# Performance work log

Hardware: AMD Instinct MI355X
Metric: run time of the kernel (lower is better)

The kernel has to match this reference:

```python
import jax, jax.numpy as jnp
import numpy as np

B, N, D, E, R = 4, 4096, 64, 131072, 64

def setup_inputs() -> dict:
    key = jax.random.key(0)
    k1, k2, k3, k4 = jax.random.split(key, 4)
    z = jax.random.normal(k1, (B, N, D), dtype=jnp.float32)
    pairs = jax.random.randint(k2, (E, 2), 0, N, dtype=jnp.int64)
    # Linear params (PyTorch convention: y = x @ W.T + b), init scale ~ 1/sqrt(fan_in)
    W1 = jax.random.normal(k3, (R, 4 * D), dtype=jnp.float32) / np.sqrt(4 * D)
    b1 = jnp.zeros((R,), dtype=jnp.float32)
    W2 = jax.random.normal(k4, (R, R), dtype=jnp.float32) / np.sqrt(R)
    b2 = jnp.zeros((R,), dtype=jnp.float32)
    return {"z": z, "pairs": pairs, "W1": W1, "b1": b1, "W2": W2, "b2": b2}

def reference(z, pairs, W1, b1, W2, b2):
    # gather endpoint embeddings: [B, E, D]
    zi = z[:, pairs[:, 0], :]
    zj = z[:, pairs[:, 1], :]
    # pair feature [B, E, 4D]: concat(zi, zj, zi-zj, zi*zj)
    pair = jnp.concatenate([zi, zj, zi - zj, zi * zj], axis=-1)
    # 2-layer MLP (dropout is identity at inference)
    h = jnp.einsum('bef,rf->ber', pair, W1) + b1
    h = jax.nn.relu(h)
    h = jnp.einsum('ber,sr->bes', h, W2) + b2
    return h
```

## Files before the change

kernel.cpp:

```cpp
#include <hip/hip_runtime.h>
#include <hip/hip_bf16.h>
#include <stdint.h>


typedef __attribute__((ext_vector_type(8))) __bf16 bf16x8;
typedef __attribute__((ext_vector_type(4))) __bf16 bf16x4;
typedef __attribute__((ext_vector_type(4))) float  f32x4;

#define E_TOT 131072
#define N_TOK 4096
#define ROWS_PER_BLOCK 512
#define NSUB 4
#define Z_ELEMS (4 * N_TOK * 64)

__global__ __launch_bounds__(256) void zcast_kernel(const float* __restrict__ z,
                                                    __bf16* __restrict__ zb)
{
    const int t = blockIdx.x * 256 + threadIdx.x;
    const float4 a = ((const float4*)z)[2 * t];
    const float4 b = ((const float4*)z)[2 * t + 1];
    bf16x8 r;
    r[0] = (__bf16)a.x; r[1] = (__bf16)a.y; r[2] = (__bf16)a.z; r[3] = (__bf16)a.w;
    r[4] = (__bf16)b.x; r[5] = (__bf16)b.y; r[6] = (__bf16)b.z; r[7] = (__bf16)b.w;
    ((bf16x8*)zb)[t] = r;
}

__device__ __forceinline__ f32x4 mfma16(bf16x8 a, bf16x8 b, f32x4 c) {
    return __builtin_amdgcn_mfma_f32_16x16x32_bf16(a, b, c, 0, 0, 0);
}

__device__ __forceinline__ bf16x8 pk8(float4 a, float4 b) {
    bf16x8 r;
    r[0] = (__bf16)a.x; r[1] = (__bf16)a.y; r[2] = (__bf16)a.z; r[3] = (__bf16)a.w;
    r[4] = (__bf16)b.x; r[5] = (__bf16)b.y; r[6] = (__bf16)b.z; r[7] = (__bf16)b.w;
    return r;
}
__device__ __forceinline__ float4 f4add(float4 a, float4 b){ return make_float4(a.x+b.x, a.y+b.y, a.z+b.z, a.w+b.w); }
__device__ __forceinline__ float4 f4sub(float4 a, float4 b){ return make_float4(a.x-b.x, a.y-b.y, a.z-b.z, a.w-b.w); }

__device__ __forceinline__ bf16x8 bmul(bf16x8 a, bf16x8 b) {
    bf16x8 r;
#pragma unroll
    for (int t = 0; t < 8; ++t)
        r[t] = (__bf16)((float)a[t] * (float)b[t]);
    return r;
}

__global__ __launch_bounds__(512, 6) void PairRelationEncoder_62775241998442_kernel(
    const __bf16* __restrict__ zw, const int* __restrict__ pairs,
    const float* __restrict__ W1, const float* __restrict__ b1,
    const float* __restrict__ W2, const float* __restrict__ b2,
    float* __restrict__ out)
{
    const int tid  = threadIdx.x;
    const int wave = tid >> 6;
    const int lane = tid & 63;
    const int x = lane & 15;
    const int g = lane >> 4;

    const int bid = (int)(blockIdx.x & 7) * 128 + ((int)blockIdx.x >> 3);
    const int m0 = bid * ROWS_PER_BLOCK;
    const int b  = m0 >> 17;
    const int e0 = m0 & (E_TOT - 1);
    const __bf16* zb = zw + ((size_t)b * N_TOK * 64);

    int2 ijv[NSUB];
#pragma unroll
    for (int st = 0; st < NSUB; ++st)
        ijv[st] = *(const int2*)(pairs + 2 * (size_t)(e0 + (st * 8 + wave) * 16 + x));

    __shared__ __bf16 w1s[64 * 192];
    __shared__ __bf16 w2s[64 * 64];
    __shared__ __bf16 h1s[8][1024];
    __shared__ float  b1s[64];
    __shared__ float  b2s[64];
    __bf16* h1w = h1s[wave];

    {
        const int part = tid >> 7;
        const int scol = tid & 63;
        const int c8b  = ((tid >> 6) & 1) * 4;
        const int cswz = (scol & 7) << 4;
        if (part < 3) {
            const float* wr = W1 + (size_t)scol * 256;
            char* dst = (char*)w1s + scol * 384;
#pragma unroll
            for (int c = 0; c < 4; ++c) {
                const int c8 = c8b + c;
                float4 p0, p1;
                if (part == 0) {
                    float4 a0 = *(const float4*)(wr + c8*8);
                    float4 a1 = *(const float4*)(wr + c8*8 + 4);
                    float4 c0 = *(const float4*)(wr + 128 + c8*8);
                    float4 c1 = *(const float4*)(wr + 128 + c8*8 + 4);
                    p0 = f4add(a0, c0); p1 = f4add(a1, c1);
                } else if (part == 1) {
                    float4 a0 = *(const float4*)(wr + 64 + c8*8);
                    float4 a1 = *(const float4*)(wr + 64 + c8*8 + 4);
                    float4 c0 = *(const float4*)(wr + 128 + c8*8);
                    float4 c1 = *(const float4*)(wr + 128 + c8*8 + 4);
                    p0 = f4sub(a0, c0); p1 = f4sub(a1, c1);
                } else {
                    p0 = *(const float4*)(wr + 192 + c8*8);
                    p1 = *(const float4*)(wr + 192 + c8*8 + 4);
                }
                *(bf16x8*)(dst + ((part * 128 + c8 * 16) ^ cswz)) = pk8(p0, p1);
            }
        } else {
            const float* wr = W2 + (size_t)scol * 64;
            char* dst = (char*)w2s + scol * 128;
#pragma unroll
            for (int c = 0; c < 4; ++c) {
                const int c8 = c8b + c;
                float4 p0 = *(const float4*)(wr + c8*8);
                float4 p1 = *(const float4*)(wr + c8*8 + 4);
                *(bf16x8*)(dst + ((c8 * 16) ^ cswz)) = pk8(p0, p1);
            }
        }
        if (tid < 16)            ((float4*)b1s)[tid]      = ((const float4*)b1)[tid];
        else if (tid < 32)       ((float4*)b2s)[tid - 16] = ((const float4*)b2)[tid - 16];
    }

    __syncthreads();

#pragma unroll
    for (int st = 0; st < NSUB; ++st) {
        const __bf16* zri = zb + (size_t)ijv[st].x * 64;
        const __bf16* zrj = zb + (size_t)ijv[st].y * 64;
        bf16x8 a0 = *(const bf16x8*)(zri + g * 8);
        bf16x8 a1 = *(const bf16x8*)(zri + 32 + g * 8);
        bf16x8 a2 = *(const bf16x8*)(zrj + g * 8);
        bf16x8 a3 = *(const bf16x8*)(zrj + 32 + g * 8);
        bf16x8 a4 = bmul(a0, a2);
        bf16x8 a5 = bmul(a1, a3);

        f32x4 acc[4];
#pragma unroll
        for (int ct = 0; ct < 4; ++ct)
            acc[ct] = *(const f32x4*)(b1s + ct * 16 + g * 4);

#pragma unroll
        for (int h = 0; h < 2; ++h) {
#pragma unroll
            for (int ct = 0; ct < 4; ++ct) {
                const int colr = ct * 16 + x;
                const int cswz = (colr & 7) << 4;
                const char* wb = (const char*)w1s + colr * 384;
                const int kb = h * 64 + g * 16;
                bf16x8 azi = *(const bf16x8*)(wb + ((kb      ) ^ cswz));
                bf16x8 azj = *(const bf16x8*)(wb + ((kb + 128) ^ cswz));
                bf16x8 apr = *(const bf16x8*)(wb + ((kb + 256) ^ cswz));
                acc[ct] = mfma16(azi, (h == 0) ? a0 : a1, acc[ct]);
                acc[ct] = mfma16(azj, (h == 0) ? a2 : a3, acc[ct]);
                acc[ct] = mfma16(apr, (h == 0) ? a4 : a5, acc[ct]);
            }
        }

#pragma unroll
        for (int ct = 0; ct < 4; ++ct) {
            bf16x4 p;
#pragma unroll
            for (int q = 0; q < 4; ++q)
                p[q] = (__bf16)fmaxf(acc[ct][q], 0.f);
            const int wo = (x * 128 + ct * 32 + g * 8) ^ ((x & 7) << 4);
            *(bf16x4*)((char*)h1w + wo) = p;
        }

        f32x4 o[4];
#pragma unroll
        for (int ct = 0; ct < 4; ++ct)
            o[ct] = *(const f32x4*)(b2s + ct * 16 + g * 4);

#pragma unroll
        for (int kk = 0; kk < 2; ++kk) {
            const int aoff = (x * 128 + kk * 64 + g * 16) ^ ((x & 7) << 4);
            const bf16x8 h1f = *(const bf16x8*)((const char*)h1w + aoff);
#pragma unroll
            for (int ct = 0; ct < 4; ++ct) {
                const int cols = ct * 16 + x;
                const bf16x8 w2f = *(const bf16x8*)((const char*)w2s + cols * 128
                                                    + ((kk * 64 + g * 16) ^ ((cols & 7) << 4)));
                o[ct] = mfma16(w2f, h1f, o[ct]);
            }
        }

        float* orow = out + ((size_t)(m0 + (st * 8 + wave) * 16 + x)) * 64;
#pragma unroll
        for (int ct = 0; ct < 4; ++ct)
            *(f32x4*)(orow + ct * 16 + g * 4) = o[ct];
    }
}

extern "C" void kernel_launch(void* const* d_in, const int* in_sizes, int n_in,
                              void* d_out, int out_size, void* d_ws, size_t ws_size,
                              hipStream_t stream) {
    const float* z     = (const float*)d_in[0];
    const int*   pairs = (const int*)  d_in[1];
    const float* W1    = (const float*)d_in[2];
    const float* b1    = (const float*)d_in[3];
    const float* W2    = (const float*)d_in[4];
    const float* b2    = (const float*)d_in[5];
    float* out = (float*)d_out;
    __bf16* zw = (__bf16*)d_ws;

    zcast_kernel<<<Z_ELEMS / (256 * 8), 256, 0, stream>>>(z, zw);

    const int total_rows = 4 * E_TOT;
    dim3 grid(total_rows / ROWS_PER_BLOCK);
    PairRelationEncoder_62775241998442_kernel<<<grid, 512, 0, stream>>>(
        zw, pairs, W1, b1, W2, b2, out);
}
```

Before: 53.72 us.

## Switch to 32x32x16 MFMA tiles and keep layer-1 activations in registers via permlane swap

Replaces the 16x16x32 bf16 MFMA tiling with 32x32x16 tiles, so each wave processes 32 pair rows per sub-step and the number of sub-steps drops from four to two. The ReLU output of layer 1 is packed with v_cvt_pk_bf16_f32 and redistributed across lanes with v_permlane32_swap, so it feeds layer 2 directly as an MFMA operand instead of going through a per-wave LDS buffer. Bias values are stored in LDS in a permuted order to match the 32x32 accumulator layout. This removes the LDS write and read of h1 and reduces per-row W1/W2 fragment reloads, but it raises register use, so the occupancy hint in launch bounds drops from 6 to 4.

```diff
diff --git a/kernel.cpp b/kernel.cpp
--- a/kernel.cpp
+++ b/kernel.cpp
@@ -3,14 +3,15 @@
 #include <stdint.h>
 
 
-typedef __attribute__((ext_vector_type(8))) __bf16 bf16x8;
-typedef __attribute__((ext_vector_type(4))) __bf16 bf16x4;
-typedef __attribute__((ext_vector_type(4))) float  f32x4;
+typedef __attribute__((ext_vector_type(8)))  __bf16 bf16x8;
+typedef __attribute__((ext_vector_type(4)))  float  f32x4;
+typedef __attribute__((ext_vector_type(16))) float  f32x16;
+typedef __attribute__((ext_vector_type(4)))  uint32_t u32x4;
 
 #define E_TOT 131072
 #define N_TOK 4096
 #define ROWS_PER_BLOCK 512
-#define NSUB 4
+#define NSUB 2
 #define Z_ELEMS (4 * N_TOK * 64)
 
 __global__ __launch_bounds__(256) void zcast_kernel(const float* __restrict__ z,
@@ -25,8 +26,8 @@
     ((bf16x8*)zb)[t] = r;
 }
 
-__device__ __forceinline__ f32x4 mfma16(bf16x8 a, bf16x8 b, f32x4 c) {
-    return __builtin_amdgcn_mfma_f32_16x16x32_bf16(a, b, c, 0, 0, 0);
+__device__ __forceinline__ f32x16 mfma32(bf16x8 a, bf16x8 b, f32x16 c) {
+    return __builtin_amdgcn_mfma_f32_32x32x16_bf16(a, b, c, 0, 0, 0);
 }
 
 __device__ __forceinline__ bf16x8 pk8(float4 a, float4 b) {
@@ -46,7 +47,45 @@
     return r;
 }
 
-__global__ __launch_bounds__(512, 6) void PairRelationEncoder_62775241998442_kernel(
+__device__ __forceinline__ uint32_t cvtpk(float lo, float hi) {
+    uint32_t w;
+    asm("v_cvt_pk_bf16_f32 %0, %1, %2" : "=v"(w) : "v"(lo), "v"(hi));
+    return w;
+}
+
+__device__ __forceinline__ void epi(const f32x16 acc, bf16x8& fA, bf16x8& fB) {
+    float v[16];
+#pragma unroll
+    for (int t = 0; t < 16; ++t) v[t] = fmaxf(acc[t], 0.f);
+    uint32_t w00 = cvtpk(v[0],  v[1]);
+    uint32_t w01 = cvtpk(v[2],  v[3]);
+    uint32_t w10 = cvtpk(v[4],  v[5]);
+    uint32_t w11 = cvtpk(v[6],  v[7]);
+    uint32_t w20 = cvtpk(v[8],  v[9]);
+    uint32_t w21 = cvtpk(v[10], v[11]);
+    uint32_t w30 = cvtpk(v[12], v[13]);
+    uint32_t w31 = cvtpk(v[14], v[15]);
+    asm("v_permlane32_swap_b32 %0, %1" : "+v"(w00), "+v"(w10));
+    asm("v_permlane32_swap_b32 %0, %1" : "+v"(w01), "+v"(w11));
+    asm("v_permlane32_swap_b32 %0, %1" : "+v"(w20), "+v"(w30));
+    asm("v_permlane32_swap_b32 %0, %1" : "+v"(w21), "+v"(w31));
+    u32x4 a = {w00, w01, w10, w11};
+    u32x4 b = {w20, w21, w30, w31};
+    fA = __builtin_bit_cast(bf16x8, a);
+    fB = __builtin_bit_cast(bf16x8, b);
+}
+
+__device__ __forceinline__ f32x16 bias_init(const float* tb, int base) {
+    f32x16 a;
+#pragma unroll
+    for (int p = 0; p < 4; ++p) {
+        f32x4 c = *(const f32x4*)(tb + base + 4 * p);
+        a[4*p+0] = c[0]; a[4*p+1] = c[1]; a[4*p+2] = c[2]; a[4*p+3] = c[3];
+    }
+    return a;
+}
+
+__global__ __launch_bounds__(512, 4) void PairRelationEncoder_62775241998442_kernel(
     const __bf16* __restrict__ zw, const int* __restrict__ pairs,
     const float* __restrict__ W1, const float* __restrict__ b1,
     const float* __restrict__ W2, const float* __restrict__ b2,
@@ -55,8 +94,8 @@
     const int tid  = threadIdx.x;
     const int wave = tid >> 6;
     const int lane = tid & 63;
-    const int x = lane & 15;
-    const int g = lane >> 4;
+    const int el = lane & 31;
+    const int hi = lane >> 5;
 
     const int bid = (int)(blockIdx.x & 7) * 128 + ((int)blockIdx.x >> 3);
     const int m0 = bid * ROWS_PER_BLOCK;
@@ -67,14 +106,12 @@
     int2 ijv[NSUB];
 #pragma unroll
     for (int st = 0; st < NSUB; ++st)
-        ijv[st] = *(const int2*)(pairs + 2 * (size_t)(e0 + (st * 8 + wave) * 16 + x));
+        ijv[st] = *(const int2*)(pairs + 2 * (size_t)(e0 + (st * 8 + wave) * 32 + el));
 
     __shared__ __bf16 w1s[64 * 192];
     __shared__ __bf16 w2s[64 * 64];
-    __shared__ __bf16 h1s[8][1024];
-    __shared__ float  b1s[64];
-    __shared__ float  b2s[64];
-    __bf16* h1w = h1s[wave];
+    __shared__ float  tb1[64];
+    __shared__ float  tb2[64];
 
     {
         const int part = tid >> 7;
@@ -117,77 +154,83 @@
                 *(bf16x8*)(dst + ((c8 * 16) ^ cswz)) = pk8(p0, p1);
             }
         }
-        if (tid < 16)            ((float4*)b1s)[tid]      = ((const float4*)b1)[tid];
-        else if (tid < 32)       ((float4*)b2s)[tid - 16] = ((const float4*)b2)[tid - 16];
+        if (tid < 64)
+            tb1[tid] = b1[((tid >> 4) & 1) * 32 + (tid & 3) + 8 * ((tid >> 2) & 3) + 4 * (tid >> 5)];
+        else if (tid < 128) {
+            const int t = tid - 64;
+            tb2[t] = b2[((t >> 4) & 1) * 32 + (t & 3) + 8 * ((t >> 2) & 3) + 4 * (t >> 5)];
+        }
     }
 
     __syncthreads();
+
+    const int sw = (el & 7) << 4;
+    const char* w1b = (const char*)w1s;
+    const char* w2b = (const char*)w2s;
 
 #pragma unroll
     for (int st = 0; st < NSUB; ++st) {
         const __bf16* zri = zb + (size_t)ijv[st].x * 64;
         const __bf16* zrj = zb + (size_t)ijv[st].y * 64;
-        bf16x8 a0 = *(const bf16x8*)(zri + g * 8);
-        bf16x8 a1 = *(const bf16x8*)(zri + 32 + g * 8);
-        bf16x8 a2 = *(const bf16x8*)(zrj + g * 8);
-        bf16x8 a3 = *(const bf16x8*)(zrj + 32 + g * 8);
-        bf16x8 a4 = bmul(a0, a2);
-        bf16x8 a5 = bmul(a1, a3);
-
-        f32x4 acc[4];
-#pragma unroll
-        for (int ct = 0; ct < 4; ++ct)
-            acc[ct] = *(const f32x4*)(b1s + ct * 16 + g * 4);
-
-#pragma unroll
-        for (int h = 0; h < 2; ++h) {
-#pragma unroll
-            for (int ct = 0; ct < 4; ++ct) {
-                const int colr = ct * 16 + x;
-                const int cswz = (colr & 7) << 4;
-                const char* wb = (const char*)w1s + colr * 384;
-                const int kb = h * 64 + g * 16;
-                bf16x8 azi = *(const bf16x8*)(wb + ((kb      ) ^ cswz));
-                bf16x8 azj = *(const bf16x8*)(wb + ((kb + 128) ^ cswz));
-                bf16x8 apr = *(const bf16x8*)(wb + ((kb + 256) ^ cswz));
-                acc[ct] = mfma16(azi, (h == 0) ? a0 : a1, acc[ct]);
-                acc[ct] = mfma16(azj, (h == 0) ? a2 : a3, acc[ct]);
-                acc[ct] = mfma16(apr, (h == 0) ? a4 : a5, acc[ct]);
-            }
-        }
-
-#pragma unroll
-        for (int ct = 0; ct < 4; ++ct) {
-            bf16x4 p;
-#pragma unroll
-            for (int q = 0; q < 4; ++q)
-                p[q] = (__bf16)fmaxf(acc[ct][q], 0.f);
-            const int wo = (x * 128 + ct * 32 + g * 8) ^ ((x & 7) << 4);
-            *(bf16x4*)((char*)h1w + wo) = p;
-        }
-
-        f32x4 o[4];
-#pragma unroll
-        for (int ct = 0; ct < 4; ++ct)
-            o[ct] = *(const f32x4*)(b2s + ct * 16 + g * 4);
-
-#pragma unroll
-        for (int kk = 0; kk < 2; ++kk) {
-            const int aoff = (x * 128 + kk * 64 + g * 16) ^ ((x & 7) << 4);
-            const bf16x8 h1f = *(const bf16x8*)((const char*)h1w + aoff);
-#pragma unroll
-            for (int ct = 0; ct < 4; ++ct) {
-                const int cols = ct * 16 + x;
-                const bf16x8 w2f = *(const bf16x8*)((const char*)w2s + cols * 128
-                                                    + ((kk * 64 + g * 16) ^ ((cols & 7) << 4)));
-                o[ct] = mfma16(w2f, h1f, o[ct]);
-            }
-        }
-
-        float* orow = out + ((size_t)(m0 + (st * 8 + wave) * 16 + x)) * 64;
-#pragma unroll
-        for (int ct = 0; ct < 4; ++ct)
-            *(f32x4*)(orow + ct * 16 + g * 4) = o[ct];
+        bf16x8 zi0 = *(const bf16x8*)(zri +      hi * 8);
+        bf16x8 zi1 = *(const bf16x8*)(zri + 16 + hi * 8);
+        bf16x8 zi2 = *(const bf16x8*)(zri + 32 + hi * 8);
+        bf16x8 zi3 = *(const bf16x8*)(zri + 48 + hi * 8);
+        bf16x8 zj0 = *(const bf16x8*)(zrj +      hi * 8);
+        bf16x8 zj1 = *(const bf16x8*)(zrj + 16 + hi * 8);
+        bf16x8 zj2 = *(const bf16x8*)(zrj + 32 + hi * 8);
+        bf16x8 zj3 = *(const bf16x8*)(zrj + 48 + hi * 8);
+
+        f32x16 acc0 = bias_init(tb1, hi * 32);
+        f32x16 acc1 = bias_init(tb1, hi * 32 + 16);
+
+#pragma unroll
+        for (int kt = 0; kt < 12; ++kt) {
+            bf16x8 bf;
+            if      (kt == 0) bf = zi0;
+            else if (kt == 1) bf = zi1;
+            else if (kt == 2) bf = zi2;
+            else if (kt == 3) bf = zi3;
+            else if (kt == 4) bf = zj0;
+            else if (kt == 5) bf = zj1;
+            else if (kt == 6) bf = zj2;
+            else if (kt == 7) bf = zj3;
+            else if (kt == 8) bf = bmul(zi0, zj0);
+            else if (kt == 9) bf = bmul(zi1, zj1);
+            else if (kt ==10) bf = bmul(zi2, zj2);
+            else              bf = bmul(zi3, zj3);
+            const int ko = (kt * 32 + hi * 16) ^ sw;
+            bf16x8 a0 = *(const bf16x8*)(w1b + (size_t)el * 384        + ko);
+            bf16x8 a1 = *(const bf16x8*)(w1b + (size_t)(32 + el) * 384 + ko);
+            acc0 = mfma32(a0, bf, acc0);
+            acc1 = mfma32(a1, bf, acc1);
+        }
+
+        bf16x8 F0, F1, F2, F3;
+        epi(acc0, F0, F1);
+        epi(acc1, F2, F3);
+
+        f32x16 o0 = bias_init(tb2, hi * 32);
+        f32x16 o1 = bias_init(tb2, hi * 32 + 16);
+
+#pragma unroll
+        for (int k2 = 0; k2 < 4; ++k2) {
+            bf16x8 pf = (k2 == 0) ? F0 : (k2 == 1) ? F1 : (k2 == 2) ? F2 : F3;
+            const int ko = (k2 * 32 + hi * 16) ^ sw;
+            bf16x8 a0 = *(const bf16x8*)(w2b + (size_t)el * 128        + ko);
+            bf16x8 a1 = *(const bf16x8*)(w2b + (size_t)(32 + el) * 128 + ko);
+            o0 = mfma32(a0, pf, o0);
+            o1 = mfma32(a1, pf, o1);
+        }
+
+        float* orow = out + ((size_t)(m0 + (st * 8 + wave) * 32 + el)) * 64;
+#pragma unroll
+        for (int p = 0; p < 4; ++p) {
+            f32x4 s0v = {o0[4*p], o0[4*p+1], o0[4*p+2], o0[4*p+3]};
+            f32x4 s1v = {o1[4*p], o1[4*p+1], o1[4*p+2], o1[4*p+3]};
+            *(f32x4*)(orow +      8 * p + 4 * hi) = s0v;
+            *(f32x4*)(orow + 32 + 8 * p + 4 * hi) = s1v;
+        }
     }
 }
 
```

New measurement: 57.92 us. 7.8% more time.
